# Optimization experiments

Measured on AMD Instinct MI355X. Metric: run time of the kernel, lower is better.

Reference implementation:

```python
import jax, jax.numpy as jnp
import numpy as np

B, N, D = 2, 2048, 128
DEPTH, RECURRENCE = 3, 3
EDGE_P = 0.03  # Bernoulli edge density -> avg degree ~61


def _p(key, shape, fan_in):
    return jax.random.normal(key, shape, dtype=jnp.float32) / np.float32(np.sqrt(fan_in))


def setup_inputs() -> dict:
    key = jax.random.key(0)
    ks = jax.random.split(key, 6)
    node = jax.random.normal(ks[0], (B, N, 1), dtype=jnp.float32)
    A = (jax.random.uniform(ks[1], (B, N, N)) < EDGE_P).astype(jnp.float32)
    edge = jax.random.uniform(ks[2], (B, N, N), dtype=jnp.float32) + 0.1  # strictly positive edge weights
    inp = {"node": node, "edge": edge, "A": A}
    # (fan_in, heads) per attention layer; last layer hardcodes heads=2, concat=False
    specs = [(1, 1), (D, 1), (D, 2)]
    for l, (fin, H) in enumerate(specs):
        kk = jax.random.split(ks[3 + l], 5)
        inp[f"Wq{l}"] = _p(kk[0], (fin, H, D), fin)
        inp[f"Wk{l}"] = _p(kk[1], (fin, H, D), fin)
        inp[f"Wv{l}"] = _p(kk[2], (fin, H, D), fin)
        inp[f"We{l}"] = _p(kk[3], (H, D), 1)  # lin_edge: edge_dim=1 -> H*D, stored as (H, D)
        inp[f"Ws{l}"] = _p(kk[4], (fin, H * D if l < DEPTH - 1 else D), fin)  # root/skip lin
    return inp


def _layer_norm(x, eps=1e-5):
    mu = x.mean(-1, keepdims=True)
    var = ((x - mu) ** 2).mean(-1, keepdims=True)
    return (x - mu) / jnp.sqrt(var + eps)


def _tconv(x, e_t, mask, Wq, Wk, Wv, We, Ws, concat):
    # PyG TransformerConv (bias removed, root_weight=True):
    #   alpha_ij = softmax_j( q_i . (k_j + W_e e_ij) / sqrt(d) ) over in-neighbors j of i
    #   out_i = sum_j alpha_ij (v_j + W_e e_ij)  (+ W_skip x_i)
    # e_ij is a scalar so W_e e_ij = e_ij * We, a rank-1 term we never materialize per-edge.
    # x: (b,n,fin); e_t[b,dst,src]; We: (H,d)
    H, d = We.shape
    q = jnp.einsum('bnf,fhd->bnhd', x, Wq)
    k = jnp.einsum('bnf,fhd->bnhd', x, Wk)
    v = jnp.einsum('bnf,fhd->bnhd', x, Wv)
    scores = jnp.einsum('bihd,bjhd->bhij', q, k)  # i=dst, j=src
    qe = jnp.einsum('bihd,hd->bhi', q, We)
    scores = (scores + qe[..., None] * e_t[:, None]) / np.float32(np.sqrt(d))
    scores = jnp.where(mask[:, None], scores, jnp.finfo(scores.dtype).min)
    alpha = jax.nn.softmax(scores, axis=-1)
    alpha = jnp.where(mask[:, None], alpha, 0.0)  # isolated dst nodes aggregate to zero
    out = jnp.einsum('bhij,bjhd->bihd', alpha, v)
    ew = jnp.einsum('bhij,bij->bhi', alpha, e_t)  # sum_j alpha * e_ij
    out = out + ew.transpose(0, 2, 1)[..., None] * We
    out = out.reshape(x.shape[0], x.shape[1], H * d) if concat else out.mean(axis=2)
    return out + x @ Ws


def reference(node, edge, A, Wq0, Wk0, Wv0, We0, Ws0, Wq1, Wk1, Wv1, We1, Ws1, Wq2, Wk2, Wv2, We2, Ws2):
    e = edge * A
    e_t = jnp.swapaxes(e, 1, 2)  # e_t[b, dst, src]  (edge_index: row=src, col=dst)
    mask = e_t != 0  # dense_to_sparse keeps nonzero entries
    layers = [
        (Wq0, Wk0, Wv0, We0, Ws0, True),
        (Wq1, Wk1, Wv1, We1, Ws1, True),
        (Wq2, Wk2, Wv2, We2, Ws2, False),
    ]
    emb = node
    for r in range(RECURRENCE):
        for l in range(DEPTH):
            if r != 0 and l == 0:
                continue
            Wq, Wk, Wv, We, Ws, concat = layers[l]
            emb = _tconv(emb, e_t, mask, Wq, Wk, Wv, We, Ws, concat)
            if l != DEPTH - 1:
                emb = jax.nn.relu(_layer_norm(emb))
    return emb  # (b, n, out_dim[-1])
```

## Files before the change

### kernel.cpp

```cpp
#include <hip/hip_runtime.h>
#include <hip/hip_bf16.h>

#define BB 2
#define NN 2048
#define DD 128
#define BN (BB*NN)
#define CAP 128
#define TD 8
#define QSTR 256
#define SSTR 128
#define INV_SQRT_D 0.08838834764831845f

typedef __attribute__((ext_vector_type(8))) short short8;
typedef __attribute__((ext_vector_type(4))) float f32x4;

__device__ inline float b2f(unsigned short u) {
    union { unsigned int i; float f; } c; c.i = (unsigned int)u << 16; return c.f;
}
__device__ inline float b2f_hi(unsigned int raw) {
    union { unsigned int i; float f; } c; c.i = raw & 0xffff0000u; return c.f;
}
__device__ inline float b2f_lo(unsigned int raw) {
    union { unsigned int i; float f; } c; c.i = raw << 16; return c.f;
}

__global__ __launch_bounds__(256) void prep(
    const float* __restrict__ A, const float* __restrict__ edge,
    const float* __restrict__ node,
    const float* __restrict__ Wq0, const float* __restrict__ Wk0,
    const float* __restrict__ Wv0, const float* __restrict__ Ws0,
    const float* __restrict__ Wq1, const float* __restrict__ Wk1,
    const float* __restrict__ Wv1, const float* __restrict__ Ws1,
    const float* __restrict__ Wq2, const float* __restrict__ Wk2,
    const float* __restrict__ Wv2, const float* __restrict__ Ws2,
    __hip_bfloat16* __restrict__ Wt1, __hip_bfloat16* __restrict__ Wt2,
    float* __restrict__ q, __hip_bfloat16* __restrict__ kA,
    __hip_bfloat16* __restrict__ vA, float* __restrict__ s,
    int* __restrict__ deg, unsigned short* __restrict__ cols,
    float* __restrict__ evals)
{
    __shared__ int   cnt[TD];
    __shared__ int   csh[TD][CAP];
    __shared__ float esh[TD][CAP];
    __shared__ float xnode[16];

    int bid = blockIdx.x;
    int tid = threadIdx.x;

    if (bid < 512) {
        int b    = bid >> 8;
        int dst0 = (bid & 255) * TD;

        if (tid < TD) cnt[tid] = 0;
        __syncthreads();

        int srcOff = tid >> 1;
        int dOff   = (tid & 1) * 4;
        const size_t base = (size_t)b * NN * NN + dst0 + dOff;

#pragma unroll 2
        for (int s0 = 0; s0 < NN; s0 += 128) {
            int src = s0 + srcOff;
            float4 a4 = *(const float4*)&A[base + (size_t)src * NN];
            float4 e4 = *(const float4*)&edge[base + (size_t)src * NN];
            int gsrc = b * NN + src;
            float av[4] = {a4.x, a4.y, a4.z, a4.w};
            float ev[4] = {e4.x, e4.y, e4.z, e4.w};
#pragma unroll
            for (int u = 0; u < 4; u++) {
                if (av[u] != 0.f) {
                    int d = dOff + u;
                    int slot = atomicAdd(&cnt[d], 1);
                    if (slot < CAP) { csh[d][slot] = gsrc; esh[d][slot] = ev[u] * av[u]; }
                }
            }
        }
        __syncthreads();

        if (tid < TD) deg[b * NN + dst0 + tid] = min(cnt[tid], CAP);
        for (int idx = tid; idx < TD * CAP; idx += 256) {
            int d = idx >> 7, i = idx & 127;
            if (i < min(cnt[d], CAP)) {
                size_t row = (size_t)(b * NN + dst0 + d);
                cols [row * CAP + i] = (unsigned short)csh[d][i];
                evals[row * CAP + i] = esh[d][i];
            }
        }
    } else if (bid < 512 + 1408) {
        int c = bid - 512;
        if (tid < DD) {
            const float *Wq, *Wk, *Wv, *Ws; __hip_bfloat16* Wt; int n, HD;
            if (c < 512) { Wq = Wq1; Wk = Wk1; Wv = Wv1; Ws = Ws1; Wt = Wt1; n = c;       HD = DD;     }
            else         { Wq = Wq2; Wk = Wk2; Wv = Wv2; Ws = Ws2; Wt = Wt2; n = c - 512; HD = 2 * DD; }
            const float* src; int ld; int col;
            if      (n < HD)     { src = Wq; col = n;          ld = HD; }
            else if (n < 2*HD)   { src = Wk; col = n - HD;     ld = HD; }
            else if (n < 3*HD)   { src = Wv; col = n - 2*HD;   ld = HD; }
            else                 { src = Ws; col = n - 3*HD;   ld = DD; }
            Wt[(size_t)n * DD + tid] = __float2bfloat16(src[(size_t)tid * ld + col]);
        }
    } else {
        int row0 = (bid - (512 + 1408)) * 16;
        if (tid < 16) xnode[tid] = node[row0 + tid];
        __syncthreads();
        for (int i = tid; i < 16 * 512; i += 256) {
            int r = i >> 9, col = i & 511;
            float xv = xnode[r];
            if (col < DD) {
                q[(size_t)(row0 + r) * QSTR + col] = xv * Wq0[col];
            } else if (col < 2*DD) {
                int lc = col - DD;
                kA[(size_t)(row0 + r) * 256 + lc] = __float2bfloat16(xv * Wk0[lc]);
            } else if (col < 3*DD) {
                int lc = col - 2*DD;
                vA[(size_t)(row0 + r) * 256 + lc] = __float2bfloat16(xv * Wv0[lc]);
            } else {
                int lc = col - 3*DD;
                s[(size_t)(row0 + r) * SSTR + lc] = xv * Ws0[lc];
            }
        }
    }
}

template<int H, bool MEANH, bool LNRELU, int NCOLS, int HDN, int KVSI, int KVSO>
__global__ __launch_bounds__(1024) void fused_attn(
    float* qio,
    const __hip_bfloat16* __restrict__ k,
    const __hip_bfloat16* __restrict__ v,
    float* sio,
    const int* __restrict__ deg,
    const unsigned short* __restrict__ cols,
    const float* __restrict__ evals, const float* __restrict__ We,
    const __hip_bfloat16* __restrict__ Wt,
    __hip_bfloat16* __restrict__ kn, __hip_bfloat16* __restrict__ vn,
    float* __restrict__ out)
{
    const int HD = H * DD;
    int wid  = threadIdx.x >> 6;
    int lane = threadIdx.x & 63;
    int row0 = blockIdx.x * 16;
    int row  = row0 + wid;
    int sub  = lane >> 4;
    int s    = lane & 15;
    int c0   = lane * 2;

    __shared__ int            jc_s[16][CAP];
    __shared__ float          ev_s[16][CAP];
    __shared__ __hip_bfloat16 xs[16][136];
    int*   jc = jc_s[wid];
    float* ev = ev_s[wid];

    int dg = min(deg[row], CAP);
    for (int m = lane; m < dg; m += 64) {
        jc[m] = (int)cols[(size_t)row * CAP + m];
        ev[m] = evals[(size_t)row * CAP + m];
    }

    float qh[H][8];
    float qeI[H];
#pragma unroll
    for (int h = 0; h < H; h++) {
        const float* qp = &qio[(size_t)row * QSTR + h * DD + s * 8];
        const float* wp = &We[h * DD + s * 8];
        float pe = 0.f;
#pragma unroll
        for (int t = 0; t < 8; t++) { qh[h][t] = qp[t]; pe += qp[t] * wp[t]; }
#pragma unroll
        for (int off = 1; off < 16; off <<= 1) pe += __shfl_xor(pe, off);
        qeI[h] = pe * INV_SQRT_D;
    }

    float l_acc[H], ew_acc[H], acc[H][2];
#pragma unroll
    for (int h = 0; h < H; h++) { l_acc[h] = 0.f; ew_acc[h] = 0.f; acc[h][0] = 0.f; acc[h][1] = 0.f; }

    for (int m0 = 0; m0 < dg; m0 += 8) {
        int   e0  = m0 + sub,       e1  = m0 + 4 + sub;
        bool  ok0 = e0 < dg,        ok1 = e1 < dg;
        int   ec0 = ok0 ? e0 : m0,  ec1 = ok1 ? e1 : m0;
        float ee0 = ev[ec0],        ee1 = ev[ec1];

        int jb[8];
#pragma unroll
        for (int es = 0; es < 8; es++) jb[es] = jc[(m0 + es < dg) ? m0 + es : m0];

        unsigned int vraw[H][8];
#pragma unroll
        for (int h = 0; h < H; h++)
#pragma unroll
            for (int es = 0; es < 8; es++)
                vraw[h][es] = *(const unsigned int*)&v[(size_t)jb[es] * KVSI + h * DD + c0];
        short8 kk0[H], kk1[H];
        {
            int j0 = jb[sub], j1 = jb[4 + sub];
#pragma unroll
            for (int h = 0; h < H; h++) {
                kk0[h] = *(const short8*)&k[(size_t)j0 * KVSI + h * DD + s * 8];
                kk1[h] = *(const short8*)&k[(size_t)j1 * KVSI + h * DD + s * 8];
            }
        }

#pragma unroll
        for (int h = 0; h < H; h++) {
            float p0 = qh[h][0]*b2f((unsigned short)kk0[h][0]) + qh[h][1]*b2f((unsigned short)kk0[h][1])
                     + qh[h][2]*b2f((unsigned short)kk0[h][2]) + qh[h][3]*b2f((unsigned short)kk0[h][3])
                     + qh[h][4]*b2f((unsigned short)kk0[h][4]) + qh[h][5]*b2f((unsigned short)kk0[h][5])
                     + qh[h][6]*b2f((unsigned short)kk0[h][6]) + qh[h][7]*b2f((unsigned short)kk0[h][7]);
            float p1 = qh[h][0]*b2f((unsigned short)kk1[h][0]) + qh[h][1]*b2f((unsigned short)kk1[h][1])
                     + qh[h][2]*b2f((unsigned short)kk1[h][2]) + qh[h][3]*b2f((unsigned short)kk1[h][3])
                     + qh[h][4]*b2f((unsigned short)kk1[h][4]) + qh[h][5]*b2f((unsigned short)kk1[h][5])
                     + qh[h][6]*b2f((unsigned short)kk1[h][6]) + qh[h][7]*b2f((unsigned short)kk1[h][7]);
#pragma unroll
            for (int off = 1; off < 16; off <<= 1) {
                p0 += __shfl_xor(p0, off);
                p1 += __shfl_xor(p1, off);
            }
            float sc0 = ok0 ? (p0 * INV_SQRT_D + qeI[h] * ee0) : -1e30f;
            float sc1 = ok1 ? (p1 * INV_SQRT_D + qeI[h] * ee1) : -1e30f;
            float a0 = __expf(fminf(sc0, 60.f));
            float a1 = __expf(fminf(sc1, 60.f));
            l_acc[h]  += a0 + a1;
            ew_acc[h] += a0 * ee0 + a1 * ee1;
            float al0[4], al1[4];
#pragma unroll
            for (int es = 0; es < 4; es++) { al0[es] = __shfl(a0, es * 16); al1[es] = __shfl(a1, es * 16); }
#pragma unroll
            for (int es = 0; es < 4; es++) {
                acc[h][0] += al0[es] * b2f_lo(vraw[h][es]) + al1[es] * b2f_lo(vraw[h][es + 4]);
                acc[h][1] += al0[es] * b2f_hi(vraw[h][es]) + al1[es] * b2f_hi(vraw[h][es + 4]);
            }
        }
    }

    float rh[H][2];
#pragma unroll
    for (int h = 0; h < H; h++) {
        float l  = l_acc[h]  + __shfl_xor(l_acc[h], 16);
        float ew = ew_acc[h] + __shfl_xor(ew_acc[h], 16);
        l  += __shfl_xor(l, 32);
        ew += __shfl_xor(ew, 32);
        float invZ = (l > 0.f) ? 1.f / l : 0.f;
        rh[h][0] = (acc[h][0] + ew * We[h * DD + c0])     * invZ;
        rh[h][1] = (acc[h][1] + ew * We[h * DD + c0 + 1]) * invZ;
    }
    float r0, r1;
    if constexpr (MEANH) {
        r0 = 0.5f * (rh[0][0] + rh[H - 1][0]);
        r1 = 0.5f * (rh[0][1] + rh[H - 1][1]);
    } else {
        r0 = rh[0][0]; r1 = rh[0][1];
    }
    float2 sk = *(const float2*)&sio[(size_t)row * SSTR + c0];
    r0 += sk.x; r1 += sk.y;

    if constexpr (LNRELU) {
        float sum = r0 + r1, sq = r0 * r0 + r1 * r1;
#pragma unroll
        for (int off = 32; off; off >>= 1) { sum += __shfl_xor(sum, off); sq += __shfl_xor(sq, off); }
        float mu  = sum * (1.f / DD);
        float var = sq * (1.f / DD) - mu * mu;
        float rs  = rsqrtf(var + 1e-5f);
        r0 = fmaxf((r0 - mu) * rs, 0.f);
        r1 = fmaxf((r1 - mu) * rs, 0.f);
    }

    if constexpr (NCOLS == 0) {
        float2 res; res.x = r0; res.y = r1;
        *(float2*)&out[(size_t)row * DD + c0] = res;
    } else {
        __hip_bfloat162 o;
        o.x = __float2bfloat16(r0);
        o.y = __float2bfloat16(r1);
        *(__hip_bfloat162*)&xs[wid][c0] = o;
        __syncthreads();

        int m16 = lane & 15, quad = lane >> 4;
        short8 a[4];
#pragma unroll
        for (int ks = 0; ks < 4; ks++)
            a[ks] = *(const short8*)&xs[m16][ks * 32 + quad * 8];

#pragma unroll 1
        for (int tile = wid; tile < NCOLS / 16; tile += 16) {
            int n0 = tile * 16;
            f32x4 pacc = {0.f, 0.f, 0.f, 0.f};
#pragma unroll
            for (int ks = 0; ks < 4; ks++) {
                const short8* bp = (const short8*)&Wt[(size_t)(n0 + m16) * DD + ks * 32 + quad * 8];
                pacc = __builtin_amdgcn_mfma_f32_16x16x32_bf16(a[ks], *bp, pacc, 0, 0, 0);
            }
            if (n0 < HDN) {
#pragma unroll
                for (int r = 0; r < 4; r++)
                    qio[(size_t)(row0 + quad * 4 + r) * QSTR + n0 + m16] = pacc[r];
            } else if (n0 < 2*HDN) {
                int lc = n0 - HDN;
#pragma unroll
                for (int r = 0; r < 4; r++)
                    kn[(size_t)(row0 + quad * 4 + r) * KVSO + lc + m16] = __float2bfloat16(pacc[r]);
            } else if (n0 < 3*HDN) {
                int lc = n0 - 2*HDN;
#pragma unroll
                for (int r = 0; r < 4; r++)
                    vn[(size_t)(row0 + quad * 4 + r) * KVSO + lc + m16] = __float2bfloat16(pacc[r]);
            } else {
                int lc = n0 - 3*HDN;
#pragma unroll
                for (int r = 0; r < 4; r++)
                    sio[(size_t)(row0 + quad * 4 + r) * SSTR + lc + m16] = pacc[r];
            }
        }
    }
}

extern "C" void kernel_launch(void* const* d_in, const int* in_sizes, int n_in,
                              void* d_out, int out_size, void* d_ws, size_t ws_size,
                              hipStream_t stream)
{
    const float* node = (const float*)d_in[0];
    const float* edge = (const float*)d_in[1];
    const float* A    = (const float*)d_in[2];
    const float* Wq[3] = {(const float*)d_in[3],  (const float*)d_in[8],  (const float*)d_in[13]};
    const float* Wk[3] = {(const float*)d_in[4],  (const float*)d_in[9],  (const float*)d_in[14]};
    const float* Wv[3] = {(const float*)d_in[5],  (const float*)d_in[10], (const float*)d_in[15]};
    const float* We[3] = {(const float*)d_in[6],  (const float*)d_in[11], (const float*)d_in[16]};
    const float* Ws[3] = {(const float*)d_in[7],  (const float*)d_in[12], (const float*)d_in[17]};

    char* p = (char*)d_ws;
    float*          q  = (float*)p;          p += (size_t)BN * QSTR * 4;
    float*          s  = (float*)p;          p += (size_t)BN * SSTR * 4;
    __hip_bfloat16* kA = (__hip_bfloat16*)p; p += (size_t)BN * 256 * 2;
    __hip_bfloat16* vA = (__hip_bfloat16*)p; p += (size_t)BN * 256 * 2;
    __hip_bfloat16* kB = (__hip_bfloat16*)p; p += (size_t)BN * 128 * 2;
    __hip_bfloat16* vB = (__hip_bfloat16*)p; p += (size_t)BN * 128 * 2;
    __hip_bfloat16* Wt1 = (__hip_bfloat16*)p; p += (size_t)512 * DD * 2;
    __hip_bfloat16* Wt2 = (__hip_bfloat16*)p; p += (size_t)896 * DD * 2;
    int*            degb = (int*)p;            p += (size_t)BN * 4;
    float*          evb  = (float*)p;          p += (size_t)BN * CAP * 4;
    unsigned short* colb = (unsigned short*)p; p += (size_t)BN * CAP * 2;

    prep<<<512 + 1408 + BN / 16, 256, 0, stream>>>(
        A, edge, node,
        Wq[0], Wk[0], Wv[0], Ws[0],
        Wq[1], Wk[1], Wv[1], Ws[1],
        Wq[2], Wk[2], Wv[2], Ws[2],
        Wt1, Wt2, q, kA, vA, s, degb, colb, evb);

    fused_attn<1, false, true, 512, 128, 256, 128><<<BN / 16, 1024, 0, stream>>>(
        q, kA, vA, s, degb, colb, evb, We[0], Wt1, kB, vB, nullptr);
    fused_attn<1, false, true, 896, 256, 128, 256><<<BN / 16, 1024, 0, stream>>>(
        q, kB, vB, s, degb, colb, evb, We[1], Wt2, kA, vA, nullptr);
    fused_attn<2, true, false, 512, 128, 256, 128><<<BN / 16, 1024, 0, stream>>>(
        q, kA, vA, s, degb, colb, evb, We[2], Wt1, kB, vB, nullptr);
    fused_attn<1, false, true, 896, 256, 128, 256><<<BN / 16, 1024, 0, stream>>>(
        q, kB, vB, s, degb, colb, evb, We[1], Wt2, kA, vA, nullptr);
    fused_attn<2, true, false, 512, 128, 256, 128><<<BN / 16, 1024, 0, stream>>>(
        q, kA, vA, s, degb, colb, evb, We[2], Wt1, kB, vB, nullptr);
    fused_attn<1, false, true, 896, 256, 128, 256><<<BN / 16, 1024, 0, stream>>>(
        q, kB, vB, s, degb, colb, evb, We[1], Wt2, kA, vA, nullptr);
    fused_attn<2, true, false, 0, 0, 256, 0><<<BN / 16, 1024, 0, stream>>>(
        q, kA, vA, s, degb, colb, evb, We[2], nullptr, nullptr, nullptr, (float*)d_out);
}
```

Baseline: 342.8 us.

## Widen adjacency-compaction tiles and split sources across blocks with atomic merge

The prep kernel's edge-list builder now has each block cover 32 destination columns over a 512-source chunk, instead of 8 columns over all sources. Each row read is 128 contiguous bytes rather than 32, which should coalesce the dense A and edge reads much better. Partial neighbour lists from the four source chunks are merged through a global atomicAdd on the degree array, which needs a memset beforehand. Neighbour order becomes nondeterministic, and the stored degree is no longer clamped to CAP if a node has more neighbours than that.

```diff
diff --git a/kernel.cpp b/kernel.cpp
--- a/kernel.cpp
+++ b/kernel.cpp
@@ -6,7 +6,7 @@
 #define DD 128
 #define BN (BB*NN)
 #define CAP 128
-#define TD 8
+#define TD 32
 #define QSTR 256
 #define SSTR 128
 #define INV_SQRT_D 0.08838834764831845f
@@ -40,6 +40,7 @@
     float* __restrict__ evals)
 {
     __shared__ int   cnt[TD];
+    __shared__ int   wbase[TD];
     __shared__ int   csh[TD][CAP];
     __shared__ float esh[TD][CAP];
     __shared__ float xnode[16];
@@ -48,22 +49,25 @@
     int tid = threadIdx.x;
 
     if (bid < 512) {
-        int b    = bid >> 8;
-        int dst0 = (bid & 255) * TD;
+        int b     = bid >> 8;
+        int r     = bid & 255;
+        int dst0  = (r >> 2) * TD;
+        int chunk = r & 3;
 
         if (tid < TD) cnt[tid] = 0;
         __syncthreads();
 
-        int srcOff = tid >> 1;
-        int dOff   = (tid & 1) * 4;
-        const size_t base = (size_t)b * NN * NN + dst0 + dOff;
+        int srcOff = tid >> 3;
+        int dOff   = (tid & 7) * 4;
+        int src0   = chunk * 512;
+        const size_t base = (size_t)b * NN * NN + (size_t)src0 * NN + dst0 + dOff;
 
 #pragma unroll 2
-        for (int s0 = 0; s0 < NN; s0 += 128) {
-            int src = s0 + srcOff;
-            float4 a4 = *(const float4*)&A[base + (size_t)src * NN];
-            float4 e4 = *(const float4*)&edge[base + (size_t)src * NN];
-            int gsrc = b * NN + src;
+        for (int s0 = 0; s0 < 512; s0 += 32) {
+            int srel = s0 + srcOff;
+            float4 a4 = *(const float4*)&A[base + (size_t)srel * NN];
+            float4 e4 = *(const float4*)&edge[base + (size_t)srel * NN];
+            int gsrc = b * NN + src0 + srel;
             float av[4] = {a4.x, a4.y, a4.z, a4.w};
             float ev[4] = {e4.x, e4.y, e4.z, e4.w};
 #pragma unroll
@@ -77,13 +81,22 @@
         }
         __syncthreads();
 
-        if (tid < TD) deg[b * NN + dst0 + tid] = min(cnt[tid], CAP);
+        if (tid < TD) {
+            int c = min(cnt[tid], CAP);
+            cnt[tid] = c;
+            wbase[tid] = atomicAdd(&deg[b * NN + dst0 + tid], c);
+        }
+        __syncthreads();
+
         for (int idx = tid; idx < TD * CAP; idx += 256) {
             int d = idx >> 7, i = idx & 127;
-            if (i < min(cnt[d], CAP)) {
-                size_t row = (size_t)(b * NN + dst0 + d);
-                cols [row * CAP + i] = (unsigned short)csh[d][i];
-                evals[row * CAP + i] = esh[d][i];
+            if (i < cnt[d]) {
+                int slot = wbase[d] + i;
+                if (slot < CAP) {
+                    size_t row = (size_t)(b * NN + dst0 + d);
+                    cols [row * CAP + slot] = (unsigned short)csh[d][i];
+                    evals[row * CAP + slot] = esh[d][i];
+                }
             }
         }
     } else if (bid < 512 + 1408) {
@@ -339,6 +352,7 @@
     float*          evb  = (float*)p;          p += (size_t)BN * CAP * 4;
     unsigned short* colb = (unsigned short*)p; p += (size_t)BN * CAP * 2;
 
+    hipMemsetAsync(degb, 0, (size_t)BN * 4, stream);
     prep<<<512 + 1408 + BN / 16, 256, 0, stream>>>(
         A, edge, node,
         Wq[0], Wk[0], Wv[0], Ws[0],
```

After: 321.8 us. 1.07x faster.
